# Kernel optimization log

Hardware: AMD Instinct MI355X
Metric: run time of the kernel (lower is better)

Reference implementation:

```python
import jax, jax.numpy as jnp
import numpy as np


def setup_inputs() -> dict:
    key = jax.random.key(0)
    k1, k2 = jax.random.split(key)
    B, D, F = 16, 512, 1500
    Q, C = 8, 1024
    latents = jax.random.normal(k1, (B, D, F), dtype=jnp.float32)
    # torch init: uniform(-1/size, 1/size)
    codebooks = jax.random.uniform(k2, (Q, C, D), dtype=jnp.float32,
                                   minval=-1.0 / C, maxval=1.0 / C)
    return {"latents": latents, "codebooks": codebooks}


def _rvq(latents, codebooks):
    B, D, F = latents.shape
    Q = codebooks.shape[0]

    def stage(residual, cb):
        # residual: [B, D, F]; cb: [C, D]
        flat = residual.transpose(0, 2, 1).reshape(-1, D)  # [N, D]
        # squared L2 distances via GEMM expansion
        dists = (jnp.sum(flat * flat, axis=1, keepdims=True)
                 - 2.0 * flat @ cb.T
                 + jnp.sum(cb * cb, axis=1))  # [N, C]
        idx = jnp.argmin(dists, axis=1)  # [N]
        q = cb[idx].reshape(B, F, D).transpose(0, 2, 1)  # [B, D, F]
        commit = jnp.mean((residual - jax.lax.stop_gradient(q)) ** 2)
        cb_loss = jnp.mean((q - jax.lax.stop_gradient(residual)) ** 2)
        new_res = residual - jax.lax.stop_gradient(q)
        return new_res, (q, idx.reshape(B, F), commit, cb_loss)

    _, (qs, codes, commits, cb_losses) = jax.lax.scan(stage, latents, codebooks)
    quantized_sum = jnp.sum(qs, axis=0)  # [B, D, F]
    # straight-through estimator
    quantized = latents + jax.lax.stop_gradient(quantized_sum - latents)
    commitment_loss = jnp.sum(commits) / Q
    codebook_loss = jnp.sum(cb_losses) / Q
    codes = jnp.transpose(codes, (1, 0, 2))  # [B, Q, F]
    return quantized, codes, commitment_loss, codebook_loss


def reference(latents, codebooks):
    return _rvq(latents, codebooks)
```

## Files before the change

### kernel.cpp

```cpp
#include <hip/hip_runtime.h>
#include <hip/hip_fp16.h>

#define B_ 16
#define D_ 512
#define F_ 1500
#define N_ (B_*F_)
#define Q_ 8
#define C_ 1024

constexpr int NBLK  = (N_ + 255) / 256;
constexpr int UPDBLK = 4 * NBLK;
constexpr int MPAD = 24064;
constexpr int FB_  = (F_ + 31) / 32;
constexpr int TILES_ = B_ * 16 * FB_;

typedef __attribute__((ext_vector_type(8))) short bf16x8;
typedef __attribute__((ext_vector_type(4))) short bf16x4;
typedef __attribute__((ext_vector_type(4))) float f32x4;

__device__ __forceinline__ short f2bf(float f) {
    unsigned u = __float_as_uint(f);
    u += 0x7FFFu + ((u >> 16) & 1u);
    return (short)(u >> 16);
}
__device__ __forceinline__ float h2f(unsigned short u) {
    __half_raw r; r.x = u; return __half2float(__half(r));
}
__device__ __forceinline__ unsigned short f2h(float f) {
    __half h = __float2half(f);
    return __half_as_ushort(h);
}

__global__ __launch_bounds__(256) void k_initT(const float* __restrict__ lat,
                                               float* __restrict__ resT,
                                               short* __restrict__ resbf) {
    __shared__ float tile[32][33];
    const int t = threadIdx.x;
    const int row = t >> 3, q4 = t & 7;
    for (int bi = blockIdx.x; bi < TILES_; bi += 1024) {
        int fb = bi % FB_, rem = bi / FB_;
        int db = rem & 15, b = rem >> 4;
        int f0 = fb * 32, d0 = db * 32;
        {
            int fbase = f0 + 4 * q4;
            const float* lp = lat + ((size_t)b * D_ + d0 + row) * F_ + fbase;
            if (fbase + 3 < F_) {
                float4 v = *(const float4*)lp;
                tile[row][4*q4+0] = v.x; tile[row][4*q4+1] = v.y;
                tile[row][4*q4+2] = v.z; tile[row][4*q4+3] = v.w;
            } else {
#pragma unroll
                for (int k = 0; k < 4; ++k)
                    tile[row][4*q4+k] = (fbase + k < F_) ? lp[k] : 0.0f;
            }
        }
        __syncthreads();
        {
            int f = f0 + row;
            if (f < F_) {
                float4 v;
                v.x = tile[4*q4+0][row]; v.y = tile[4*q4+1][row];
                v.z = tile[4*q4+2][row]; v.w = tile[4*q4+3][row];
                size_t o = ((size_t)(b * F_ + f)) * D_ + d0 + 4 * q4;
                *(float4*)(resT + o) = v;
                bf16x4 s;
                s[0] = f2bf(v.x); s[1] = f2bf(v.y); s[2] = f2bf(v.z); s[3] = f2bf(v.w);
                *(bf16x4*)(resbf + o) = s;
            }
        }
        __syncthreads();
    }
}

__global__ void k_cbh(const float* __restrict__ cb, short* __restrict__ cbh) {
    for (int g = blockIdx.x * 256 + threadIdx.x; g < Q_ * C_ * D_ / 8; g += 512 * 256) {
        size_t base = (size_t)g * 8;
        float4 a = *(const float4*)(cb + base);
        float4 b = *(const float4*)(cb + base + 4);
        bf16x8 o;
        o[0]=f2bf(a.x); o[1]=f2bf(a.y); o[2]=f2bf(a.z); o[3]=f2bf(a.w);
        o[4]=f2bf(b.x); o[5]=f2bf(b.y); o[6]=f2bf(b.z); o[7]=f2bf(b.w);
        *(bf16x8*)(cbh + base) = o;
    }
}

__global__ void k_cbnormP(const float* __restrict__ cb, float* __restrict__ Hq) {
#pragma clang fp contract(off)
    int wid = blockIdx.x * 256 + threadIdx.x;
    const float* p = cb + (size_t)wid * D_;
    float L[4];
#pragma unroll
    for (int l = 0; l < 4; ++l) {
        const float* pl = p + l * 128;
        float r[8];
#pragma unroll
        for (int j = 0; j < 8; ++j) { float x = pl[j]; r[j] = x * x; }
        for (int i = 8; i < 128; i += 8) {
#pragma unroll
            for (int j = 0; j < 8; ++j) { float x = pl[i + j]; r[j] = r[j] + x * x; }
        }
        L[l] = ((r[0] + r[1]) + (r[2] + r[3])) + ((r[4] + r[5]) + (r[6] + r[7]));
    }
    Hq[wid] = (L[0] + L[1]) + (L[2] + L[3]);
}

__global__ void k_rownorm4(const float* __restrict__ resT, float* __restrict__ Sp) {
#pragma clang fp contract(off)
    int n = blockIdx.x * 256 + threadIdx.x;
    if (n >= N_) return;
#pragma unroll
    for (int l = 0; l < 4; ++l) {
        const float* p = resT + (size_t)n * D_ + l * 128;
        float r[8];
#pragma unroll
        for (int j = 0; j < 8; ++j) { float x = p[j]; r[j] = x * x; }
        for (int i = 8; i < 128; i += 8) {
#pragma unroll
            for (int j = 0; j < 8; ++j) { float x = p[i + j]; r[j] = r[j] + x * x; }
        }
        Sp[(size_t)l * N_ + n] = ((r[0] + r[1]) + (r[2] + r[3])) + ((r[4] + r[5]) + (r[6] + r[7]));
    }
}

#define LSTR 80
__global__ __launch_bounds__(256) void k_gemm2(
        const short* __restrict__ resbf, const short* __restrict__ cbh,
        const float* __restrict__ resT, const float* __restrict__ cb,
        const float* __restrict__ Hq, const float* __restrict__ Sp,
        int* __restrict__ codes, int q) {
#pragma clang fp contract(off)
    __shared__ short xh[64 * LSTR];
    __shared__ short ch[128 * LSTR];
    __shared__ float smin[64][2];
    __shared__ float bminG[64];
    __shared__ unsigned lcnt[64];
    __shared__ unsigned slots[64][16];
    __shared__ unsigned witems[1024];
    __shared__ unsigned long long rkeyL[64];
    __shared__ int fbrows[64];
    __shared__ unsigned wcnt_s, fbcnt_s;

    const int t = threadIdx.x, l = t & 63, w = t >> 6;
    const int wr = w >> 1, wc = w & 1;
    const int n0 = blockIdx.x * 64;
    const short* cbhq = cbh + (size_t)q * C_ * D_;
    const float* Hqq = Hq + (size_t)q * C_;
    const float* cbq = cb + (size_t)q * ((size_t)C_ * D_);

    if (t < 64) { bminG[t] = 3.4e38f; lcnt[t] = 0; rkeyL[t] = ~0ull; }
    if (t == 0) { wcnt_s = 0; fbcnt_s = 0; }

    for (int c0 = 0; c0 < C_; c0 += 128) {
        f32x4 acc[2][4];
#pragma unroll
        for (int i = 0; i < 2; ++i)
#pragma unroll
            for (int j = 0; j < 4; ++j) { acc[i][j][0]=0.f; acc[i][j][1]=0.f; acc[i][j][2]=0.f; acc[i][j][3]=0.f; }

        for (int kc = 0; kc < D_; kc += 64) {
            __syncthreads();
            {
                int idx = t; int nn = idx >> 3, d8 = idx & 7;
                *(bf16x8*)(&xh[nn * LSTR + d8 * 8]) =
                    *(const bf16x8*)(resbf + (size_t)(n0 + nn) * D_ + kc + d8 * 8);
                idx = 256 + t; nn = idx >> 3; d8 = idx & 7;
                *(bf16x8*)(&xh[nn * LSTR + d8 * 8]) =
                    *(const bf16x8*)(resbf + (size_t)(n0 + nn) * D_ + kc + d8 * 8);
            }
#pragma unroll
            for (int p = 0; p < 4; ++p) {
                int idx = p * 256 + t;
                int cr = idx >> 3, d8 = idx & 7;
                *(bf16x8*)(&ch[cr * LSTR + d8 * 8]) =
                    *(const bf16x8*)(cbhq + (size_t)(c0 + cr) * D_ + kc + d8 * 8);
            }
            __syncthreads();

#pragma unroll
            for (int kf = 0; kf < 2; ++kf) {
                const int ko = kf * 32 + (l >> 4) * 8;
                bf16x8 ah[2], bh[4];
#pragma unroll
                for (int i = 0; i < 2; ++i)
                    ah[i] = *(const bf16x8*)(&xh[(wr * 32 + i * 16 + (l & 15)) * LSTR + ko]);
#pragma unroll
                for (int j = 0; j < 4; ++j)
                    bh[j] = *(const bf16x8*)(&ch[(wc * 64 + j * 16 + (l & 15)) * LSTR + ko]);
#pragma unroll
                for (int i = 0; i < 2; ++i)
#pragma unroll
                    for (int j = 0; j < 4; ++j)
                        acc[i][j] = __builtin_amdgcn_mfma_f32_16x16x32_bf16(ah[i], bh[j], acc[i][j], 0, 0, 0);
            }
        }

        float hv[4];
#pragma unroll
        for (int j = 0; j < 4; ++j) hv[j] = Hqq[c0 + wc * 64 + j * 16 + (l & 15)];

#pragma unroll
        for (int i = 0; i < 2; ++i)
#pragma unroll
            for (int r = 0; r < 4; ++r) {
                float vm = hv[0] - 2.0f * acc[i][0][r];
#pragma unroll
                for (int j = 1; j < 4; ++j) vm = fminf(vm, hv[j] - 2.0f * acc[i][j][r]);
                vm = fminf(vm, __shfl_xor(vm, 1, 64));
                vm = fminf(vm, __shfl_xor(vm, 2, 64));
                vm = fminf(vm, __shfl_xor(vm, 4, 64));
                vm = fminf(vm, __shfl_xor(vm, 8, 64));
                if ((l & 15) == 0) smin[wr * 32 + i * 16 + (l >> 4) * 4 + r][wc] = vm;
            }
        __syncthreads();
        if (t < 64) bminG[t] = fminf(bminG[t], fminf(smin[t][0], smin[t][1]));
        __syncthreads();
#pragma unroll
        for (int i = 0; i < 2; ++i)
#pragma unroll
            for (int j = 0; j < 4; ++j)
#pragma unroll
                for (int r = 0; r < 4; ++r) {
                    int row = wr * 32 + i * 16 + (l >> 4) * 4 + r;
                    float v = hv[j] - 2.0f * acc[i][j][r];
                    if (v <= bminG[row] + 1.6e-3f) {
                        unsigned pos = atomicAdd(&lcnt[row], 1u);
                        if (pos < 16) {
                            unsigned c = (unsigned)(c0 + wc * 64 + j * 16 + (l & 15));
                            slots[row][pos] = ((unsigned)f2h(v) << 16) | c;
                        }
                    }
                }
    }
    __syncthreads();

    if (t < 64) {
        int n = n0 + t;
        float thr = bminG[t] + 1.5e-3f;
        unsigned lc = lcnt[t];
        if (lc > 16u) {
            unsigned fp = atomicAdd(&fbcnt_s, 1u);
            fbrows[fp] = t;
        } else {
            int cnt = 0, c1 = -1;
            for (unsigned s = 0; s < lc; ++s) {
                unsigned e = slots[t][s];
                if (h2f((unsigned short)(e >> 16)) <= thr) { ++cnt; if (cnt == 1) c1 = (int)(e & 0x3FFu); }
            }
            if (cnt == 1) {
                codes[(size_t)q * N_ + n] = c1;
            } else {
                for (unsigned s = 0; s < lc; ++s) {
                    unsigned e = slots[t][s];
                    if (h2f((unsigned short)(e >> 16)) <= thr) {
                        unsigned pos = atomicAdd(&wcnt_s, 1u);
                        witems[pos] = ((unsigned)t << 10) | (e & 0x3FFu);
                    }
                }
            }
        }
    }
    __syncthreads();

    {
        unsigned wn = wcnt_s;
        for (unsigned i = t; i < wn; i += 256) {
            unsigned e = witems[i];
            int lr = (int)(e >> 10), c = (int)(e & 0x3FFu);
            int n = n0 + lr;
            float S = (Sp[n] + Sp[N_ + n]) + (Sp[2 * N_ + n] + Sp[3 * N_ + n]);
            const float* xr = resT + (size_t)n * D_;
            const float* cr = cbq + (size_t)c * D_;
            float A = 0.0f;
#pragma unroll 8
            for (int d = 0; d < D_; ++d) A = fmaf(xr[d], cr[d], A);
            float v = (S - 2.0f * A) + Hqq[c];
            unsigned long long key = ((unsigned long long)__float_as_uint(v) << 32) | (unsigned)c;
            atomicMin(&rkeyL[lr], key);
        }
    }
    __syncthreads();
    if (t < 64 && rkeyL[t] != ~0ull)
        codes[(size_t)q * N_ + n0 + t] = (int)(rkeyL[t] & 0x3FFull);

    {
        unsigned fn = fbcnt_s;
        for (unsigned fi = w; fi < fn; fi += 4) {
            int n = n0 + fbrows[fi];
            float S = (Sp[n] + Sp[N_ + n]) + (Sp[2 * N_ + n] + Sp[3 * N_ + n]);
            const float4* xr4 = (const float4*)(resT + (size_t)n * D_);
            float mn = 3.4e38f;
            for (int rep = 0; rep < 16; ++rep) {
                int c = l + rep * 64;
                const float4* cr4 = (const float4*)(cbq + (size_t)c * D_);
                float a0 = 0.f, a1 = 0.f, a2 = 0.f, a3 = 0.f;
#pragma unroll 4
                for (int d4 = 0; d4 < 128; ++d4) {
                    float4 xv = xr4[d4], cv = cr4[d4];
                    a0 = fmaf(xv.x, cv.x, a0); a1 = fmaf(xv.y, cv.y, a1);
                    a2 = fmaf(xv.z, cv.z, a2); a3 = fmaf(xv.w, cv.w, a3);
                }
                float v = (S - 2.0f * ((a0 + a1) + (a2 + a3))) + Hqq[c];
                mn = fminf(mn, v);
            }
            for (int off = 32; off; off >>= 1) mn = fminf(mn, __shfl_xor(mn, off, 64));
            const float thr2 = mn + 6e-4f;
            float bv = 3.4e38f; int bc = 0x7fffffff;
            const float* xr = resT + (size_t)n * D_;
            for (int rep = 0; rep < 16; ++rep) {
                int c = l + rep * 64;
                const float4* cr4 = (const float4*)(cbq + (size_t)c * D_);
                float a0 = 0.f, a1 = 0.f, a2 = 0.f, a3 = 0.f;
#pragma unroll 4
                for (int d4 = 0; d4 < 128; ++d4) {
                    float4 xv = xr4[d4], cv = cr4[d4];
                    a0 = fmaf(xv.x, cv.x, a0); a1 = fmaf(xv.y, cv.y, a1);
                    a2 = fmaf(xv.z, cv.z, a2); a3 = fmaf(xv.w, cv.w, a3);
                }
                float vap = (S - 2.0f * ((a0 + a1) + (a2 + a3))) + Hqq[c];
                if (vap <= thr2) {
                    const float* cr = cbq + (size_t)c * D_;
                    float A = 0.0f;
#pragma unroll 8
                    for (int d = 0; d < D_; ++d) A = fmaf(xr[d], cr[d], A);
                    float v = (S - 2.0f * A) + Hqq[c];
                    if (v < bv || (v == bv && c < bc)) { bv = v; bc = c; }
                }
            }
            for (int off = 32; off; off >>= 1) {
                float ov = __shfl_xor(bv, off, 64);
                int oc = __shfl_xor(bc, off, 64);
                if (ov < bv || (ov == bv && oc < bc)) { bv = ov; bc = oc; }
            }
            if (l == 0) codes[(size_t)q * N_ + n] = bc;
        }
    }
}

__global__ __launch_bounds__(256) void k_upd(
        float* __restrict__ resT, short* __restrict__ resbf,
        const float* __restrict__ cb, const int* __restrict__ codes,
        float* __restrict__ Sp, double* __restrict__ part, int q) {
#pragma clang fp contract(off)
    int seg = blockIdx.x / NBLK;
    int nb  = blockIdx.x % NBLK;
    int n = nb * 256 + threadIdx.x;
    float L = 0.0f;
    if (n < N_) {
        int idx = codes[(size_t)q * N_ + n];
        const float4* cr4 = (const float4*)(cb + ((size_t)q * C_ + idx) * D_ + seg * 128);
        float4* rp4 = (float4*)(resT + (size_t)n * D_ + seg * 128);
        short* rb = resbf + (size_t)n * D_ + seg * 128;
        float r8[8];
#pragma unroll
        for (int k = 0; k < 16; ++k) {
            float4 a = rp4[2*k], b = rp4[2*k+1];
            float4 ca = cr4[2*k], cb2 = cr4[2*k+1];
            float v0 = a.x - ca.x, v1 = a.y - ca.y, v2 = a.z - ca.z, v3 = a.w - ca.w;
            float v4 = b.x - cb2.x, v5 = b.y - cb2.y, v6 = b.z - cb2.z, v7 = b.w - cb2.w;
            rp4[2*k]   = float4{v0, v1, v2, v3};
            rp4[2*k+1] = float4{v4, v5, v6, v7};
            bf16x8 o;
            o[0]=f2bf(v0); o[1]=f2bf(v1); o[2]=f2bf(v2); o[3]=f2bf(v3);
            o[4]=f2bf(v4); o[5]=f2bf(v5); o[6]=f2bf(v6); o[7]=f2bf(v7);
            *(bf16x8*)(rb + 8*k) = o;
            if (k == 0) {
                r8[0]=v0*v0; r8[1]=v1*v1; r8[2]=v2*v2; r8[3]=v3*v3;
                r8[4]=v4*v4; r8[5]=v5*v5; r8[6]=v6*v6; r8[7]=v7*v7;
            } else {
                r8[0]=r8[0]+v0*v0; r8[1]=r8[1]+v1*v1; r8[2]=r8[2]+v2*v2; r8[3]=r8[3]+v3*v3;
                r8[4]=r8[4]+v4*v4; r8[5]=r8[5]+v5*v5; r8[6]=r8[6]+v6*v6; r8[7]=r8[7]+v7*v7;
            }
        }
        L = ((r8[0] + r8[1]) + (r8[2] + r8[3])) + ((r8[4] + r8[5]) + (r8[6] + r8[7]));
        Sp[(size_t)seg * N_ + n] = L;
    }
    double s = (double)L;
#pragma unroll
    for (int off = 32; off; off >>= 1) s += __shfl_down(s, off, 64);
    __shared__ double sred[4];
    int lane = threadIdx.x & 63, wv = threadIdx.x >> 6;
    if (lane == 0) sred[wv] = s;
    __syncthreads();
    if (threadIdx.x == 0)
        part[(size_t)q * UPDBLK + blockIdx.x] = sred[0] + sred[1] + sred[2] + sred[3];
}

__global__ __launch_bounds__(256) void k_out0T(const float* __restrict__ lat,
                                               const float* __restrict__ resT,
                                               float* __restrict__ out) {
    __shared__ float tile[32][33];
    const int t = threadIdx.x;
    const int row = t >> 3, q4 = t & 7;
    for (int bi = blockIdx.x; bi < TILES_; bi += 1024) {
        int fb = bi % FB_, rem = bi / FB_;
        int db = rem & 15, b = rem >> 4;
        int f0 = fb * 32, d0 = db * 32;
        {
            int f = f0 + row;
            if (f < F_) {
                float4 v = *(const float4*)(resT + ((size_t)(b * F_ + f)) * D_ + d0 + 4 * q4);
                tile[4*q4+0][row] = v.x; tile[4*q4+1][row] = v.y;
                tile[4*q4+2][row] = v.z; tile[4*q4+3][row] = v.w;
            }
        }
        __syncthreads();
        {
            int fbase = f0 + 4 * q4;
            size_t o = ((size_t)b * D_ + d0 + row) * F_ + fbase;
            if (fbase + 3 < F_) {
                float4 lv = *(const float4*)(lat + o);
                float4 v;
                v.x = lv.x - tile[row][4*q4+0]; v.y = lv.y - tile[row][4*q4+1];
                v.z = lv.z - tile[row][4*q4+2]; v.w = lv.w - tile[row][4*q4+3];
                *(float4*)(out + o) = v;
            } else {
#pragma unroll
                for (int k = 0; k < 4; ++k)
                    if (fbase + k < F_) out[o + k] = lat[o + k] - tile[row][4*q4+k];
            }
        }
        __syncthreads();
    }
}

__global__ void k_codes(const int* __restrict__ codes, float* __restrict__ out1) {
    int bi = blockIdx.x;
    int q = bi & 7, b = bi >> 3;
    for (int f = threadIdx.x; f < F_; f += 256)
        out1[(size_t)bi * F_ + f] = (float)codes[(size_t)q * N_ + (size_t)b * F_ + f];
}

__global__ void k_loss(const double* __restrict__ part, float* __restrict__ out2) {
    double s = 0.0;
    for (int i = threadIdx.x; i < Q_ * UPDBLK; i += 256) s += part[i];
#pragma unroll
    for (int off = 32; off; off >>= 1) s += __shfl_down(s, off, 64);
    __shared__ double red[4];
    int lane = threadIdx.x & 63, wv = threadIdx.x >> 6;
    if (lane == 0) red[wv] = s;
    __syncthreads();
    if (threadIdx.x == 0) {
        double tot = red[0] + red[1] + red[2] + red[3];
        float val = (float)(tot / ((double)Q_ * (double)B_ * (double)D_ * (double)F_));
        out2[0] = val;
        out2[1] = val;
    }
}

extern "C" void kernel_launch(void* const* d_in, const int* in_sizes, int n_in,
                              void* d_out, int out_size, void* d_ws, size_t ws_size,
                              hipStream_t stream) {
    const float* lat = (const float*)d_in[0];
    const float* cb  = (const float*)d_in[1];
    char* ws = (char*)d_ws;
    float*  resT  = (float*)(ws);
    short*  resbf = (short*)(ws + 49283072);
    short*  cbh   = (short*)(ws + 73924608);
    int*    codes = (int*)(ws + 82313216);
    float*  Hq    = (float*)(ws + 83081216);
    float*  Sp    = (float*)(ws + 83113984);
    double* part  = (double*)(ws + 83497984);
    float* out = (float*)d_out;

    hipLaunchKernelGGL(k_initT,    dim3(1024), dim3(256), 0, stream, lat, resT, resbf);
    hipLaunchKernelGGL(k_cbh,      dim3(512), dim3(256), 0, stream, cb, cbh);
    hipLaunchKernelGGL(k_cbnormP,  dim3(Q_ * C_ / 256), dim3(256), 0, stream, cb, Hq);
    hipLaunchKernelGGL(k_rownorm4, dim3(NBLK), dim3(256), 0, stream, resT, Sp);

    for (int q = 0; q < Q_; ++q) {
        hipLaunchKernelGGL(k_gemm2, dim3(N_ / 64), dim3(256), 0, stream,
                           resbf, cbh, resT, cb, Hq, Sp, codes, q);
        hipLaunchKernelGGL(k_upd,   dim3(UPDBLK), dim3(256), 0, stream,
                           resT, resbf, cb, codes, Sp, part, q);
    }

    hipLaunchKernelGGL(k_out0T, dim3(1024), dim3(256), 0, stream, lat, resT, out);
    hipLaunchKernelGGL(k_codes, dim3(B_ * Q_), dim3(256), 0, stream, codes, out + 12288000);
    hipLaunchKernelGGL(k_loss,  dim3(1), dim3(256), 0, stream, part, out + 12480000);
}
```

Before: 1.283 ms.

## Fuse argmin GEMM and residual update into one per-stage kernel with 32-row tiles

Merges the distance GEMM/argmin kernel and the residual-update kernel into a single k_stage kernel per quantizer stage. Codes stay in shared memory and the same block updates its residual rows, which saves a launch and a global round-trip for the codes. The row tile shrinks from 64 to 32, doubling the block count, so each block does half the MFMA work per codebook tile and reloads the codebook tile for fewer rows. That lowers data reuse in exchange for more parallelism, and only 128 threads do the update phase.

Result: slower. 1.481 ms (+15.5%).

```diff
diff --git a/kernel.cpp b/kernel.cpp
--- a/kernel.cpp
+++ b/kernel.cpp
@@ -9,10 +9,10 @@
 #define C_ 1024
 
 constexpr int NBLK  = (N_ + 255) / 256;
-constexpr int UPDBLK = 4 * NBLK;
 constexpr int MPAD = 24064;
 constexpr int FB_  = (F_ + 31) / 32;
 constexpr int TILES_ = B_ * 16 * FB_;
+constexpr int SBLK_ = N_ / 32;
 
 typedef __attribute__((ext_vector_type(8))) short bf16x8;
 typedef __attribute__((ext_vector_type(4))) short bf16x4;
@@ -123,47 +123,43 @@
 }
 
 #define LSTR 80
-__global__ __launch_bounds__(256) void k_gemm2(
-        const short* __restrict__ resbf, const short* __restrict__ cbh,
-        const float* __restrict__ resT, const float* __restrict__ cb,
-        const float* __restrict__ Hq, const float* __restrict__ Sp,
-        int* __restrict__ codes, int q) {
+__global__ __launch_bounds__(256) void k_stage(
+        const short* __restrict__ cbh, float* __restrict__ resT,
+        short* __restrict__ resbf, const float* __restrict__ cb,
+        const float* __restrict__ Hq, float* __restrict__ Sp,
+        int* __restrict__ codes, double* __restrict__ part, int q) {
 #pragma clang fp contract(off)
-    __shared__ short xh[64 * LSTR];
+    __shared__ short xh[32 * LSTR];
     __shared__ short ch[128 * LSTR];
-    __shared__ float smin[64][2];
-    __shared__ float bminG[64];
-    __shared__ unsigned lcnt[64];
-    __shared__ unsigned slots[64][16];
-    __shared__ unsigned witems[1024];
-    __shared__ unsigned long long rkeyL[64];
-    __shared__ int fbrows[64];
+    __shared__ float smin[32][2];
+    __shared__ float bminG[32];
+    __shared__ unsigned lcnt[32];
+    __shared__ unsigned slots[32][16];
+    __shared__ unsigned witems[512];
+    __shared__ unsigned long long rkeyL[32];
+    __shared__ int fbrows[32];
+    __shared__ int codeL[32];
     __shared__ unsigned wcnt_s, fbcnt_s;
 
     const int t = threadIdx.x, l = t & 63, w = t >> 6;
     const int wr = w >> 1, wc = w & 1;
-    const int n0 = blockIdx.x * 64;
+    const int n0 = blockIdx.x * 32;
     const short* cbhq = cbh + (size_t)q * C_ * D_;
     const float* Hqq = Hq + (size_t)q * C_;
     const float* cbq = cb + (size_t)q * ((size_t)C_ * D_);
 
-    if (t < 64) { bminG[t] = 3.4e38f; lcnt[t] = 0; rkeyL[t] = ~0ull; }
+    if (t < 32) { bminG[t] = 3.4e38f; lcnt[t] = 0; rkeyL[t] = ~0ull; }
     if (t == 0) { wcnt_s = 0; fbcnt_s = 0; }
 
     for (int c0 = 0; c0 < C_; c0 += 128) {
-        f32x4 acc[2][4];
-#pragma unroll
-        for (int i = 0; i < 2; ++i)
-#pragma unroll
-            for (int j = 0; j < 4; ++j) { acc[i][j][0]=0.f; acc[i][j][1]=0.f; acc[i][j][2]=0.f; acc[i][j][3]=0.f; }
+        f32x4 acc[4];
+#pragma unroll
+        for (int j = 0; j < 4; ++j) { acc[j][0]=0.f; acc[j][1]=0.f; acc[j][2]=0.f; acc[j][3]=0.f; }
 
         for (int kc = 0; kc < D_; kc += 64) {
             __syncthreads();
             {
-                int idx = t; int nn = idx >> 3, d8 = idx & 7;
-                *(bf16x8*)(&xh[nn * LSTR + d8 * 8]) =
-                    *(const bf16x8*)(resbf + (size_t)(n0 + nn) * D_ + kc + d8 * 8);
-                idx = 256 + t; nn = idx >> 3; d8 = idx & 7;
+                int nn = t >> 3, d8 = t & 7;
                 *(bf16x8*)(&xh[nn * LSTR + d8 * 8]) =
                     *(const bf16x8*)(resbf + (size_t)(n0 + nn) * D_ + kc + d8 * 8);
             }
@@ -179,18 +175,14 @@
 #pragma unroll
             for (int kf = 0; kf < 2; ++kf) {
                 const int ko = kf * 32 + (l >> 4) * 8;
-                bf16x8 ah[2], bh[4];
-#pragma unroll
-                for (int i = 0; i < 2; ++i)
-                    ah[i] = *(const bf16x8*)(&xh[(wr * 32 + i * 16 + (l & 15)) * LSTR + ko]);
+                bf16x8 ah = *(const bf16x8*)(&xh[(wr * 16 + (l & 15)) * LSTR + ko]);
+                bf16x8 bh[4];
 #pragma unroll
                 for (int j = 0; j < 4; ++j)
                     bh[j] = *(const bf16x8*)(&ch[(wc * 64 + j * 16 + (l & 15)) * LSTR + ko]);
 #pragma unroll
-                for (int i = 0; i < 2; ++i)
-#pragma unroll
-                    for (int j = 0; j < 4; ++j)
-                        acc[i][j] = __builtin_amdgcn_mfma_f32_16x16x32_bf16(ah[i], bh[j], acc[i][j], 0, 0, 0);
+                for (int j = 0; j < 4; ++j)
+                    acc[j] = __builtin_amdgcn_mfma_f32_16x16x32_bf16(ah, bh[j], acc[j], 0, 0, 0);
             }
         }
 
@@ -199,42 +191,37 @@
         for (int j = 0; j < 4; ++j) hv[j] = Hqq[c0 + wc * 64 + j * 16 + (l & 15)];
 
 #pragma unroll
-        for (int i = 0; i < 2; ++i)
+        for (int r = 0; r < 4; ++r) {
+            float vm = hv[0] - 2.0f * acc[0][r];
+#pragma unroll
+            for (int j = 1; j < 4; ++j) vm = fminf(vm, hv[j] - 2.0f * acc[j][r]);
+            vm = fminf(vm, __shfl_xor(vm, 1, 64));
+            vm = fminf(vm, __shfl_xor(vm, 2, 64));
+            vm = fminf(vm, __shfl_xor(vm, 4, 64));
+            vm = fminf(vm, __shfl_xor(vm, 8, 64));
+            if ((l & 15) == 0) smin[wr * 16 + (l >> 4) * 4 + r][wc] = vm;
+        }
+        __syncthreads();
+        if (t < 32) bminG[t] = fminf(bminG[t], fminf(smin[t][0], smin[t][1]));
+        __syncthreads();
+#pragma unroll
+        for (int j = 0; j < 4; ++j)
 #pragma unroll
             for (int r = 0; r < 4; ++r) {
-                float vm = hv[0] - 2.0f * acc[i][0][r];
-#pragma unroll
-                for (int j = 1; j < 4; ++j) vm = fminf(vm, hv[j] - 2.0f * acc[i][j][r]);
-                vm = fminf(vm, __shfl_xor(vm, 1, 64));
-                vm = fminf(vm, __shfl_xor(vm, 2, 64));
-                vm = fminf(vm, __shfl_xor(vm, 4, 64));
-                vm = fminf(vm, __shfl_xor(vm, 8, 64));
-                if ((l & 15) == 0) smin[wr * 32 + i * 16 + (l >> 4) * 4 + r][wc] = vm;
-            }
-        __syncthreads();
-        if (t < 64) bminG[t] = fminf(bminG[t], fminf(smin[t][0], smin[t][1]));
-        __syncthreads();
-#pragma unroll
-        for (int i = 0; i < 2; ++i)
-#pragma unroll
-            for (int j = 0; j < 4; ++j)
-#pragma unroll
-                for (int r = 0; r < 4; ++r) {
-                    int row = wr * 32 + i * 16 + (l >> 4) * 4 + r;
-                    float v = hv[j] - 2.0f * acc[i][j][r];
-                    if (v <= bminG[row] + 1.6e-3f) {
-                        unsigned pos = atomicAdd(&lcnt[row], 1u);
-                        if (pos < 16) {
-                            unsigned c = (unsigned)(c0 + wc * 64 + j * 16 + (l & 15));
-                            slots[row][pos] = ((unsigned)f2h(v) << 16) | c;
-                        }
+                int row = wr * 16 + (l >> 4) * 4 + r;
+                float v = hv[j] - 2.0f * acc[j][r];
+                if (v <= bminG[row] + 1.6e-3f) {
+                    unsigned pos = atomicAdd(&lcnt[row], 1u);
+                    if (pos < 16) {
+                        unsigned c = (unsigned)(c0 + wc * 64 + j * 16 + (l & 15));
+                        slots[row][pos] = ((unsigned)f2h(v) << 16) | c;
                     }
                 }
-    }
-    __syncthreads();
-
-    if (t < 64) {
-        int n = n0 + t;
+            }
+    }
+    __syncthreads();
+
+    if (t < 32) {
         float thr = bminG[t] + 1.5e-3f;
         unsigned lc = lcnt[t];
         if (lc > 16u) {
@@ -247,8 +234,9 @@
                 if (h2f((unsigned short)(e >> 16)) <= thr) { ++cnt; if (cnt == 1) c1 = (int)(e & 0x3FFu); }
             }
             if (cnt == 1) {
-                codes[(size_t)q * N_ + n] = c1;
+                codeL[t] = c1;
             } else {
+                codeL[t] = -1;
                 for (unsigned s = 0; s < lc; ++s) {
                     unsigned e = slots[t][s];
                     if (h2f((unsigned short)(e >> 16)) <= thr) {
@@ -279,13 +267,13 @@
         }
     }
     __syncthreads();
-    if (t < 64 && rkeyL[t] != ~0ull)
-        codes[(size_t)q * N_ + n0 + t] = (int)(rkeyL[t] & 0x3FFull);
+    if (t < 32 && codeL[t] < 0) codeL[t] = (int)(rkeyL[t] & 0x3FFull);
 
     {
         unsigned fn = fbcnt_s;
         for (unsigned fi = w; fi < fn; fi += 4) {
-            int n = n0 + fbrows[fi];
+            int lr = fbrows[fi];
+            int n = n0 + lr;
             float S = (Sp[n] + Sp[N_ + n]) + (Sp[2 * N_ + n] + Sp[3 * N_ + n]);
             const float4* xr4 = (const float4*)(resT + (size_t)n * D_);
             float mn = 3.4e38f;
@@ -331,22 +319,17 @@
                 int oc = __shfl_xor(bc, off, 64);
                 if (ov < bv || (ov == bv && oc < bc)) { bv = ov; bc = oc; }
             }
-            if (l == 0) codes[(size_t)q * N_ + n] = bc;
-        }
-    }
-}
-
-__global__ __launch_bounds__(256) void k_upd(
-        float* __restrict__ resT, short* __restrict__ resbf,
-        const float* __restrict__ cb, const int* __restrict__ codes,
-        float* __restrict__ Sp, double* __restrict__ part, int q) {
-#pragma clang fp contract(off)
-    int seg = blockIdx.x / NBLK;
-    int nb  = blockIdx.x % NBLK;
-    int n = nb * 256 + threadIdx.x;
+            if (l == 0) codeL[lr] = bc;
+        }
+    }
+    __syncthreads();
+    if (t < 32) codes[(size_t)q * N_ + n0 + t] = codeL[t];
+
     float L = 0.0f;
-    if (n < N_) {
-        int idx = codes[(size_t)q * N_ + n];
+    if (t < 128) {
+        int lr = t >> 2, seg = t & 3;
+        int n = n0 + lr;
+        int idx = codeL[lr];
         const float4* cr4 = (const float4*)(cb + ((size_t)q * C_ + idx) * D_ + seg * 128);
         float4* rp4 = (float4*)(resT + (size_t)n * D_ + seg * 128);
         short* rb = resbf + (size_t)n * D_ + seg * 128;
@@ -382,7 +365,7 @@
     if (lane == 0) sred[wv] = s;
     __syncthreads();
     if (threadIdx.x == 0)
-        part[(size_t)q * UPDBLK + blockIdx.x] = sred[0] + sred[1] + sred[2] + sred[3];
+        part[(size_t)q * SBLK_ + blockIdx.x] = sred[0] + sred[1] + sred[2] + sred[3];
 }
 
 __global__ __launch_bounds__(256) void k_out0T(const float* __restrict__ lat,
@@ -432,7 +415,7 @@
 
 __global__ void k_loss(const double* __restrict__ part, float* __restrict__ out2) {
     double s = 0.0;
-    for (int i = threadIdx.x; i < Q_ * UPDBLK; i += 256) s += part[i];
+    for (int i = threadIdx.x; i < Q_ * SBLK_; i += 256) s += part[i];
 #pragma unroll
     for (int off = 32; off; off >>= 1) s += __shfl_down(s, off, 64);
     __shared__ double red[4];
@@ -468,10 +451,8 @@
     hipLaunchKernelGGL(k_rownorm4, dim3(NBLK), dim3(256), 0, stream, resT, Sp);
 
     for (int q = 0; q < Q_; ++q) {
-        hipLaunchKernelGGL(k_gemm2, dim3(N_ / 64), dim3(256), 0, stream,
-                           resbf, cbh, resT, cb, Hq, Sp, codes, q);
-        hipLaunchKernelGGL(k_upd,   dim3(UPDBLK), dim3(256), 0, stream,
-                           resT, resbf, cb, codes, Sp, part, q);
+        hipLaunchKernelGGL(k_stage, dim3(SBLK_), dim3(256), 0, stream,
+                           cbh, resT, resbf, cb, Hq, Sp, codes, part, q);
     }
 
     hipLaunchKernelGGL(k_out0T, dim3(1024), dim3(256), 0, stream, lat, resT, out);
```

## Fuse residual update into GEMM-argmin stage kernel and register-prefetch tiles

Applied to the files above, without the earlier changes.

Merges the per-stage distance/argmin kernel and the residual-update kernel into one launch per stage. Each 64-row block now computes its codes into shared memory, then updates the residual, bf16 copy, row norms and loss partials for those rows directly, without a separate kernel reading codes back from global memory. Also adds register double-buffering so the next K-chunk of residual and codebook tiles is loaded from global memory while the current chunk's MFMAs run. The update phase now uses 375 blocks instead of about 376 larger-grid blocks, and the prefetch adds registers, which may lower occupancy.

Result: faster. 1.154 ms (-10.1%).

```diff
diff --git a/kernel.cpp b/kernel.cpp
--- a/kernel.cpp
+++ b/kernel.cpp
@@ -9,10 +9,9 @@
 #define C_ 1024
 
 constexpr int NBLK  = (N_ + 255) / 256;
-constexpr int UPDBLK = 4 * NBLK;
-constexpr int MPAD = 24064;
 constexpr int FB_  = (F_ + 31) / 32;
 constexpr int TILES_ = B_ * 16 * FB_;
+constexpr int SBLK_ = N_ / 64;
 
 typedef __attribute__((ext_vector_type(8))) short bf16x8;
 typedef __attribute__((ext_vector_type(4))) short bf16x4;
@@ -123,11 +122,11 @@
 }
 
 #define LSTR 80
-__global__ __launch_bounds__(256) void k_gemm2(
-        const short* __restrict__ resbf, const short* __restrict__ cbh,
-        const float* __restrict__ resT, const float* __restrict__ cb,
-        const float* __restrict__ Hq, const float* __restrict__ Sp,
-        int* __restrict__ codes, int q) {
+__global__ __launch_bounds__(256) void k_stage(
+        const short* __restrict__ cbh, float* __restrict__ resT,
+        short* __restrict__ resbf, const float* __restrict__ cb,
+        const float* __restrict__ Hq, float* __restrict__ Sp,
+        int* __restrict__ codes, double* __restrict__ part, int q) {
 #pragma clang fp contract(off)
     __shared__ short xh[64 * LSTR];
     __shared__ short ch[128 * LSTR];
@@ -138,11 +137,13 @@
     __shared__ unsigned witems[1024];
     __shared__ unsigned long long rkeyL[64];
     __shared__ int fbrows[64];
+    __shared__ int codeL[64];
     __shared__ unsigned wcnt_s, fbcnt_s;
 
     const int t = threadIdx.x, l = t & 63, w = t >> 6;
     const int wr = w >> 1, wc = w & 1;
     const int n0 = blockIdx.x * 64;
+    const int nn = t >> 3, d8 = t & 7;
     const short* cbhq = cbh + (size_t)q * C_ * D_;
     const float* Hqq = Hq + (size_t)q * C_;
     const float* cbq = cb + (size_t)q * ((size_t)C_ * D_);
@@ -150,6 +151,15 @@
     if (t < 64) { bminG[t] = 3.4e38f; lcnt[t] = 0; rkeyL[t] = ~0ull; }
     if (t == 0) { wcnt_s = 0; fbcnt_s = 0; }
 
+    bf16x8 rxa, rxb, rc[4];
+    {
+        rxa = *(const bf16x8*)(resbf + (size_t)(n0 + nn) * D_ + d8 * 8);
+        rxb = *(const bf16x8*)(resbf + (size_t)(n0 + 32 + nn) * D_ + d8 * 8);
+#pragma unroll
+        for (int p = 0; p < 4; ++p)
+            rc[p] = *(const bf16x8*)(cbhq + (size_t)(32 * p + nn) * D_ + d8 * 8);
+    }
+
     for (int c0 = 0; c0 < C_; c0 += 128) {
         f32x4 acc[2][4];
 #pragma unroll
@@ -159,22 +169,24 @@
 
         for (int kc = 0; kc < D_; kc += 64) {
             __syncthreads();
+            *(bf16x8*)(&xh[nn * LSTR + d8 * 8]) = rxa;
+            *(bf16x8*)(&xh[(32 + nn) * LSTR + d8 * 8]) = rxb;
+#pragma unroll
+            for (int p = 0; p < 4; ++p)
+                *(bf16x8*)(&ch[(32 * p + nn) * LSTR + d8 * 8]) = rc[p];
+            __syncthreads();
+
             {
-                int idx = t; int nn = idx >> 3, d8 = idx & 7;
-                *(bf16x8*)(&xh[nn * LSTR + d8 * 8]) =
-                    *(const bf16x8*)(resbf + (size_t)(n0 + nn) * D_ + kc + d8 * 8);
-                idx = 256 + t; nn = idx >> 3; d8 = idx & 7;
-                *(bf16x8*)(&xh[nn * LSTR + d8 * 8]) =
-                    *(const bf16x8*)(resbf + (size_t)(n0 + nn) * D_ + kc + d8 * 8);
-            }
-#pragma unroll
-            for (int p = 0; p < 4; ++p) {
-                int idx = p * 256 + t;
-                int cr = idx >> 3, d8 = idx & 7;
-                *(bf16x8*)(&ch[cr * LSTR + d8 * 8]) =
-                    *(const bf16x8*)(cbhq + (size_t)(c0 + cr) * D_ + kc + d8 * 8);
-            }
-            __syncthreads();
+                int nkc = kc + 64, nc0 = c0;
+                if (nkc == D_) { nkc = 0; nc0 = c0 + 128; }
+                if (nc0 < C_) {
+                    rxa = *(const bf16x8*)(resbf + (size_t)(n0 + nn) * D_ + nkc + d8 * 8);
+                    rxb = *(const bf16x8*)(resbf + (size_t)(n0 + 32 + nn) * D_ + nkc + d8 * 8);
+#pragma unroll
+                    for (int p = 0; p < 4; ++p)
+                        rc[p] = *(const bf16x8*)(cbhq + (size_t)(nc0 + 32 * p + nn) * D_ + nkc + d8 * 8);
+                }
+            }
 
 #pragma unroll
             for (int kf = 0; kf < 2; ++kf) {
@@ -234,7 +246,6 @@
     __syncthreads();
 
     if (t < 64) {
-        int n = n0 + t;
         float thr = bminG[t] + 1.5e-3f;
         unsigned lc = lcnt[t];
         if (lc > 16u) {
@@ -247,8 +258,9 @@
                 if (h2f((unsigned short)(e >> 16)) <= thr) { ++cnt; if (cnt == 1) c1 = (int)(e & 0x3FFu); }
             }
             if (cnt == 1) {
-                codes[(size_t)q * N_ + n] = c1;
+                codeL[t] = c1;
             } else {
+                codeL[t] = -1;
                 for (unsigned s = 0; s < lc; ++s) {
                     unsigned e = slots[t][s];
                     if (h2f((unsigned short)(e >> 16)) <= thr) {
@@ -279,13 +291,13 @@
         }
     }
     __syncthreads();
-    if (t < 64 && rkeyL[t] != ~0ull)
-        codes[(size_t)q * N_ + n0 + t] = (int)(rkeyL[t] & 0x3FFull);
+    if (t < 64 && codeL[t] < 0) codeL[t] = (int)(rkeyL[t] & 0x3FFull);
 
     {
         unsigned fn = fbcnt_s;
         for (unsigned fi = w; fi < fn; fi += 4) {
-            int n = n0 + fbrows[fi];
+            int lr = fbrows[fi];
+            int n = n0 + lr;
             float S = (Sp[n] + Sp[N_ + n]) + (Sp[2 * N_ + n] + Sp[3 * N_ + n]);
             const float4* xr4 = (const float4*)(resT + (size_t)n * D_);
             float mn = 3.4e38f;
@@ -331,22 +343,17 @@
                 int oc = __shfl_xor(bc, off, 64);
                 if (ov < bv || (ov == bv && oc < bc)) { bv = ov; bc = oc; }
             }
-            if (l == 0) codes[(size_t)q * N_ + n] = bc;
-        }
-    }
-}
-
-__global__ __launch_bounds__(256) void k_upd(
-        float* __restrict__ resT, short* __restrict__ resbf,
-        const float* __restrict__ cb, const int* __restrict__ codes,
-        float* __restrict__ Sp, double* __restrict__ part, int q) {
-#pragma clang fp contract(off)
-    int seg = blockIdx.x / NBLK;
-    int nb  = blockIdx.x % NBLK;
-    int n = nb * 256 + threadIdx.x;
+            if (l == 0) codeL[lr] = bc;
+        }
+    }
+    __syncthreads();
+    if (t < 64) codes[(size_t)q * N_ + n0 + t] = codeL[t];
+
     float L = 0.0f;
-    if (n < N_) {
-        int idx = codes[(size_t)q * N_ + n];
+    {
+        int lr = t >> 2, seg = t & 3;
+        int n = n0 + lr;
+        int idx = codeL[lr];
         const float4* cr4 = (const float4*)(cb + ((size_t)q * C_ + idx) * D_ + seg * 128);
         float4* rp4 = (float4*)(resT + (size_t)n * D_ + seg * 128);
         short* rb = resbf + (size_t)n * D_ + seg * 128;
@@ -382,7 +389,7 @@
     if (lane == 0) sred[wv] = s;
     __syncthreads();
     if (threadIdx.x == 0)
-        part[(size_t)q * UPDBLK + blockIdx.x] = sred[0] + sred[1] + sred[2] + sred[3];
+        part[(size_t)q * SBLK_ + blockIdx.x] = sred[0] + sred[1] + sred[2] + sred[3];
 }
 
 __global__ __launch_bounds__(256) void k_out0T(const float* __restrict__ lat,
@@ -432,7 +439,7 @@
 
 __global__ void k_loss(const double* __restrict__ part, float* __restrict__ out2) {
     double s = 0.0;
-    for (int i = threadIdx.x; i < Q_ * UPDBLK; i += 256) s += part[i];
+    for (int i = threadIdx.x; i < Q_ * SBLK_; i += 256) s += part[i];
 #pragma unroll
     for (int off = 32; off; off >>= 1) s += __shfl_down(s, off, 64);
     __shared__ double red[4];
@@ -468,10 +475,8 @@
     hipLaunchKernelGGL(k_rownorm4, dim3(NBLK), dim3(256), 0, stream, resT, Sp);
 
     for (int q = 0; q < Q_; ++q) {
-        hipLaunchKernelGGL(k_gemm2, dim3(N_ / 64), dim3(256), 0, stream,
-                           resbf, cbh, resT, cb, Hq, Sp, codes, q);
-        hipLaunchKernelGGL(k_upd,   dim3(UPDBLK), dim3(256), 0, stream,
-                           resT, resbf, cb, codes, Sp, part, q);
+        hipLaunchKernelGGL(k_stage, dim3(SBLK_), dim3(256), 0, stream,
+                           cbh, resT, resbf, cb, Hq, Sp, codes, part, q);
     }
 
     hipLaunchKernelGGL(k_out0T, dim3(1024), dim3(256), 0, stream, lat, resT, out);
```
